# Performance work log

Hardware: AMD Instinct MI355X
Metric: run time of the kernel (lower is better)

## Reference

```python
import jax, jax.numpy as jnp
import numpy as np

N = 160000          # n_users + n_entities (amazon-book scale)
E = 5_120_000       # nonzeros in A_in (avg degree 32)
DIMS = [64, 64, 32, 16]  # conv_dim_list 64-32-16 on top of embed_dim 64


def setup_inputs() -> dict:
    key = jax.random.key(0)
    ks = jax.random.split(key, 4 + 4 * (len(DIMS) - 1))
    inp = {
        "ego": jax.random.normal(ks[0], (N, DIMS[0]), dtype=jnp.float32) * 0.1,
        "edge_row": jax.random.randint(ks[1], (E,), 0, N, dtype=jnp.int32),
        "edge_col": jax.random.randint(ks[2], (E,), 0, N, dtype=jnp.int32),
        # normalized-adjacency-like values
        "edge_val": jax.random.uniform(ks[3], (E,), dtype=jnp.float32) / 32.0,
    }
    ki = 4
    for i in range(len(DIMS) - 1):
        din, dout = DIMS[i], DIMS[i + 1]
        scale = 1.0 / np.sqrt(din)
        inp[f"W1_{i}"] = jax.random.normal(ks[ki], (din, dout), dtype=jnp.float32) * scale
        inp[f"b1_{i}"] = jnp.zeros((dout,), dtype=jnp.float32)
        inp[f"W2_{i}"] = jax.random.normal(ks[ki + 1], (din, dout), dtype=jnp.float32) * scale
        inp[f"b2_{i}"] = jnp.zeros((dout,), dtype=jnp.float32)
        ki += 2
    return inp


def _leaky(x):
    return jnp.where(x >= 0, x, 0.01 * x)  # nn.LeakyReLU default slope


def _l2norm(x):
    # F.normalize(x, p=2, dim=1), eps=1e-12
    n = jnp.sqrt(jnp.sum(x * x, axis=1, keepdims=True))
    return x / jnp.maximum(n, 1e-12)


def _spmm(row, col, val, x):
    # sparse A_in (COO) @ x : gather neighbor rows, scale, scatter-add
    msgs = val[:, None] * x[col]                      # [E, d]
    return jax.ops.segment_sum(msgs, row, num_segments=N)  # [N, d]


def reference(ego, edge_row, edge_col, edge_val,
              W1_0, b1_0, W2_0, b2_0,
              W1_1, b1_1, W2_1, b2_1,
              W1_2, b1_2, W2_2, b2_2):
    params = [(W1_0, b1_0, W2_0, b2_0),
              (W1_1, b1_1, W2_1, b2_1),
              (W1_2, b1_2, W2_2, b2_2)]
    x = ego
    all_embed = [x]
    for W1, b1, W2, b2 in params:
        side = _spmm(edge_row, edge_col, edge_val, x)         # A_in @ ego
        sum_emb = _leaky((x + side) @ W1 + b1)                # linear1 branch
        bi_emb = _leaky((x * side) @ W2 + b2)                 # linear2 branch
        x = sum_emb + bi_emb                                  # (dropout = identity, eval)
        all_embed.append(_l2norm(x))
    return jnp.concatenate(all_embed, axis=1)                 # [N, 64+64+32+16]
```

## Files before the change

kernel.cpp:

```cpp
#include <hip/hip_runtime.h>
#include <hip/hip_bf16.h>

#define LEAKY(v) ((v) >= 0.0f ? (v) : 0.01f * (v))

typedef int iv4 __attribute__((ext_vector_type(4)));
typedef unsigned short us4 __attribute__((ext_vector_type(4)));
typedef short s8v __attribute__((ext_vector_type(8)));
typedef float f4 __attribute__((ext_vector_type(4)));

constexpr int SH = 9;
constexpr int RPB = 1 << SH;
constexpr int NBMAX = 320;
constexpr int CHUNK = 6144;

__device__ __forceinline__ unsigned short f2bf(float v) {
  unsigned u = __float_as_uint(v);
  return (unsigned short)((u + 0x7fffu + ((u >> 16) & 1u)) >> 16);
}
__device__ __forceinline__ float bf2f(unsigned short h) {
  return __uint_as_float((unsigned)h << 16);
}

__global__ void k_init(const float* __restrict__ ego, float* __restrict__ out,
                       unsigned short* __restrict__ xh, int n) {
  int tid = blockIdx.x * blockDim.x + threadIdx.x;
  int total = n * 16;
  int stride = gridDim.x * blockDim.x;
  for (int t = tid; t < total; t += stride) {
    int r = t >> 4, c = (t & 15) * 4;
    float4 v = *(const float4*)(ego + (size_t)r * 64 + c);
    *(float4*)(out + (size_t)r * 176 + c) = v;
    if (xh) {
      us4 h;
      h.x = f2bf(v.x); h.y = f2bf(v.y); h.z = f2bf(v.z); h.w = f2bf(v.w);
      *(us4*)(xh + (size_t)r * 64 + c) = h;
    }
  }
}

__global__ void __launch_bounds__(256) k_hist(const int* __restrict__ erow,
                                              int* __restrict__ bcnt, int E, int nb) {
  __shared__ int h[NBMAX];
  for (int i = threadIdx.x; i < NBMAX; i += 256) h[i] = 0;
  __syncthreads();
  int tid = blockIdx.x * blockDim.x + threadIdx.x;
  int stride = gridDim.x * blockDim.x;
  for (int e = tid; e < E; e += stride) atomicAdd(&h[erow[e] >> SH], 1);
  __syncthreads();
  for (int b = threadIdx.x; b < nb; b += 256)
    if (h[b]) atomicAdd(&bcnt[b], h[b]);
}

__global__ void k_scanb(const int* __restrict__ bcnt, int* __restrict__ boff,
                        int* __restrict__ bcur, int* __restrict__ rp,
                        int nb, int n, int E) {
  int l = threadIdx.x;
  constexpr int PB = NBMAX / 64;
  int local[PB];
  int s = 0;
  int base = l * PB;
  for (int j = 0; j < PB; ++j) {
    int b = base + j;
    int c = (b < nb) ? bcnt[b] : 0;
    local[j] = c;
    s += c;
  }
  int incl = s;
  for (int d = 1; d < 64; d <<= 1) {
    int v = __shfl_up(incl, d);
    if (l >= d) incl += v;
  }
  int ex = incl - s;
  for (int j = 0; j < PB; ++j) {
    int b = base + j;
    if (b <= nb) { boff[b] = ex; bcur[b] = ex; }
    ex += local[j];
  }
  if (l == 63) boff[nb] = incl;
  if (l == 0) rp[n] = E;
}

__global__ void __launch_bounds__(256) k_bucket(
    const int* __restrict__ erow, const int* __restrict__ ecol,
    const float* __restrict__ ev, int* __restrict__ bcur,
    int2* __restrict__ bkt, int E, int nb) {
  __shared__ int hist[NBMAX];
  __shared__ int excl[NBMAX + 1];
  __shared__ int curl[NBMAX];
  __shared__ int gbase[NBMAX];
  __shared__ int2 skv[CHUNK];
  int base = blockIdx.x * CHUNK;
  int cnt = min(CHUNK, E - base);

  for (int i = threadIdx.x; i < NBMAX; i += 256) hist[i] = 0;
  __syncthreads();
  for (int i = threadIdx.x; i < cnt; i += 256)
    atomicAdd(&hist[erow[base + i] >> SH], 1);
  __syncthreads();

  if (threadIdx.x < 64) {
    int l = threadIdx.x;
    constexpr int PB = NBMAX / 64;
    int lsum[PB];
    int s = 0;
    for (int j = 0; j < PB; ++j) { lsum[j] = hist[l * PB + j]; s += lsum[j]; }
    int incl = s;
    for (int d = 1; d < 64; d <<= 1) {
      int v = __shfl_up(incl, d);
      if (l >= d) incl += v;
    }
    int ex = incl - s;
    for (int j = 0; j < PB; ++j) { excl[l * PB + j] = ex; ex += lsum[j]; }
    if (l == 63) excl[NBMAX] = incl;
  }
  __syncthreads();

  for (int b = threadIdx.x; b < nb; b += 256) {
    curl[b] = 0;
    int c = hist[b];
    if (c) gbase[b] = atomicAdd(&bcur[b], c);
  }
  __syncthreads();

  for (int i = threadIdx.x; i < cnt; i += 256) {
    int r = erow[base + i];
    int b = r >> SH;
    int lr = r & (RPB - 1);
    int slot = excl[b] + atomicAdd(&curl[b], 1);
    int2 p;
    p.x = (lr << 18) | ecol[base + i];
    p.y = __float_as_int(ev[base + i]);
    skv[slot] = p;
  }
  __syncthreads();

  for (int s = threadIdx.x; s < cnt; s += 256) {
    int lo = 0, hi = nb;
    while (hi - lo > 1) {
      int mid = (lo + hi) >> 1;
      if (excl[mid] <= s) lo = mid; else hi = mid;
    }
    bkt[gbase[lo] + (s - excl[lo])] = skv[s];
  }
}

__global__ void __launch_bounds__(512) k_bsort(
    const int* __restrict__ boff, const int2* __restrict__ bkt,
    int2* __restrict__ cv, int* __restrict__ rp, int n) {
  __shared__ int cnt[RPB];
  __shared__ int sc[RPB];
  __shared__ int exs[RPB];
  __shared__ int cur[RPB];
  int b = blockIdx.x;
  int off = boff[b];
  int m = boff[b + 1] - off;
  int t = threadIdx.x;

  cnt[t] = 0;
  __syncthreads();
  for (int i = t; i < m; i += 512) atomicAdd(&cnt[bkt[off + i].x >> 18], 1);
  __syncthreads();
  sc[t] = cnt[t];
  __syncthreads();
  for (int o = 1; o < RPB; o <<= 1) {
    int v = (t >= o) ? sc[t - o] : 0;
    __syncthreads();
    sc[t] += v;
    __syncthreads();
  }
  int ex = sc[t] - cnt[t];
  exs[t] = ex;
  cur[t] = 0;
  int row = (b << SH) + t;
  if (row < n) rp[row] = off + ex;
  __syncthreads();
  for (int i = t; i < m; i += 512) {
    int2 p = bkt[off + i];
    int lr = p.x >> 18;
    int pos = exs[lr] + atomicAdd(&cur[lr], 1);
    int2 q;
    q.x = p.x & 0x3FFFF;
    q.y = p.y;
    cv[off + pos] = q;
  }
}

template <int DIN, bool BF>
__global__ void __launch_bounds__(256, 8) k_gam(
    const int* __restrict__ rp, const int2* __restrict__ cv,
    const unsigned short* __restrict__ xh, const float* __restrict__ xin,
    unsigned* __restrict__ amp, int n) {
  int row = (int)((blockIdx.x * (unsigned)blockDim.x + threadIdx.x) >> 6);
  int lane = threadIdx.x & 63;
  if (row >= n) return;

  int f = lane & (DIN - 1);
  int beg = rp[row], end = rp[row + 1];

  float xv = (lane < DIN) ? xin[(size_t)row * 176 + lane] : 0.0f;

#define GATH(col) (BF ? bf2f(xh[(unsigned)((col) * 64 + f)]) \
                      : xin[(size_t)(col) * 176 + f])
  float acc = 0.0f;
  int e = beg;
  if ((e & 1) && e < end) {
    int2 q = cv[e];
    acc = fmaf(__int_as_float(q.y), GATH(q.x), acc);
    ++e;
  }
  for (; e + 4 <= end; e += 4) {
    iv4 a = *(const iv4*)(cv + e);
    iv4 b = *(const iv4*)(cv + e + 2);
    float g0 = GATH(a.x);
    float g1 = GATH(a.z);
    float g2 = GATH(b.x);
    float g3 = GATH(b.z);
    acc = fmaf(__int_as_float(a.y), g0, acc);
    acc = fmaf(__int_as_float(a.w), g1, acc);
    acc = fmaf(__int_as_float(b.y), g2, acc);
    acc = fmaf(__int_as_float(b.w), g3, acc);
  }
  for (; e + 2 <= end; e += 2) {
    iv4 a = *(const iv4*)(cv + e);
    float g0 = GATH(a.x);
    float g1 = GATH(a.z);
    acc = fmaf(__int_as_float(a.y), g0, acc);
    acc = fmaf(__int_as_float(a.w), g1, acc);
  }
  if (e < end) {
    int2 q = cv[e];
    acc = fmaf(__int_as_float(q.y), GATH(q.x), acc);
  }
#undef GATH

  if (lane < DIN) {
    float a = xv + acc, m = xv * acc;
    amp[(size_t)row * 64 + lane] = (unsigned)f2bf(a) | ((unsigned)f2bf(m) << 16);
  }
}

template <int DIN, int DOUT>
__global__ void __launch_bounds__(256) k_xf(
    const unsigned* __restrict__ amp,
    const float* __restrict__ W1, const float* __restrict__ b1,
    const float* __restrict__ W2, const float* __restrict__ b2,
    float* __restrict__ outp, unsigned short* __restrict__ xh, int n) {
  constexpr int ROWB = DIN * 2;
  constexpr int RMASK = (ROWB / 16) - 1;
  constexpr int NTC = DOUT / 16;
  __shared__ unsigned short sA[64 * DIN];
  __shared__ unsigned short sM[64 * DIN];
  __shared__ unsigned short sW1[DOUT * DIN];
  __shared__ unsigned short sW2[DOUT * DIN];

  int row0 = blockIdx.x * 64;

  constexpr int PAIRS = DIN / 2;
  for (int i = threadIdx.x; i < 64 * PAIRS; i += 256) {
    int r = i / PAIRS, fp = (i - r * PAIRS) * 2;
    unsigned lo = 0, hi = 0;
    if (row0 + r < n) {
      uint2 q = *(const uint2*)(amp + (size_t)(row0 + r) * 64 + fp);
      lo = (q.x & 0xffffu) | ((q.y & 0xffffu) << 16);
      hi = (q.x >> 16) | (q.y & 0xffff0000u);
    }
    int boff = r * ROWB + ((fp * 2) ^ ((r & RMASK) << 4));
    *(unsigned*)((char*)sA + boff) = lo;
    *(unsigned*)((char*)sM + boff) = hi;
  }
  for (int i = threadIdx.x; i < DIN * DOUT; i += 256) {
    int k = i / DOUT, c = i - k * DOUT;
    int boff = c * ROWB + ((k * 2) ^ ((c & RMASK) << 4));
    *(unsigned short*)((char*)sW1 + boff) = f2bf(W1[i]);
    *(unsigned short*)((char*)sW2 + boff) = f2bf(W2[i]);
  }
  __syncthreads();

  int w = threadIdx.x >> 6, l = threadIdx.x & 63;
  int tr = w;

  f4 acc1[NTC], acc2[NTC];
#pragma unroll
  for (int tc = 0; tc < NTC; ++tc) {
    acc1[tc] = (f4){0.0f, 0.0f, 0.0f, 0.0f};
    acc2[tc] = (f4){0.0f, 0.0f, 0.0f, 0.0f};
  }

#pragma unroll
  for (int k0 = 0; k0 < DIN; k0 += 32) {
    int ra = tr * 16 + (l & 15);
    int inb = (k0 + (l >> 4) * 8) * 2;
    s8v af = *(const s8v*)((const char*)sA + ra * ROWB + (inb ^ ((ra & RMASK) << 4)));
    s8v mf = *(const s8v*)((const char*)sM + ra * ROWB + (inb ^ ((ra & RMASK) << 4)));
#pragma unroll
    for (int tc = 0; tc < NTC; ++tc) {
      int rc = tc * 16 + (l & 15);
      int wb = rc * ROWB + (inb ^ ((rc & RMASK) << 4));
      s8v w1 = *(const s8v*)((const char*)sW1 + wb);
      s8v w2 = *(const s8v*)((const char*)sW2 + wb);
      acc1[tc] = __builtin_amdgcn_mfma_f32_16x16x32_bf16(af, w1, acc1[tc], 0, 0, 0);
      acc2[tc] = __builtin_amdgcn_mfma_f32_16x16x32_bf16(mf, w2, acc2[tc], 0, 0, 0);
    }
  }

#pragma unroll
  for (int tc = 0; tc < NTC; ++tc) {
    int c = tc * 16 + (l & 15);
    float bb1 = b1[c], bb2 = b2[c];
#pragma unroll
    for (int j = 0; j < 4; ++j) {
      int r = tr * 16 + (l >> 4) * 4 + j;
      if (row0 + r < n) {
        float v1 = acc1[tc][j] + bb1;
        float v2 = acc2[tc][j] + bb2;
        float xn = LEAKY(v1) + LEAKY(v2);
        outp[(size_t)(row0 + r) * 176 + c] = xn;
        if (xh) xh[(size_t)(row0 + r) * 64 + c] = f2bf(xn);
      }
    }
  }
}

__global__ void __launch_bounds__(256) k_norm(float* out, int n) {
  int row = (int)((blockIdx.x * (unsigned)blockDim.x + threadIdx.x) >> 6);
  int lane = threadIdx.x & 63;
  if (row >= n) return;
  float* r = out + (size_t)row * 176;
  float a = r[64 + lane];
  float b = (lane < 48) ? r[128 + lane] : 0.0f;
  float sa = a * a;
  float sb_ = (lane < 32) ? b * b : 0.0f;
  float sc = (lane >= 32 && lane < 48) ? b * b : 0.0f;
#pragma unroll
  for (int off = 32; off; off >>= 1) {
    sa += __shfl_xor(sa, off);
    sb_ += __shfl_xor(sb_, off);
    sc += __shfl_xor(sc, off);
  }
  float ia = 1.0f / fmaxf(sqrtf(sa), 1e-12f);
  float ib = 1.0f / fmaxf(sqrtf(sb_), 1e-12f);
  float ic = 1.0f / fmaxf(sqrtf(sc), 1e-12f);
  r[64 + lane] = a * ia;
  if (lane < 48) r[128 + lane] = b * ((lane < 32) ? ib : ic);
}

extern "C" void kernel_launch(void* const* d_in, const int* in_sizes, int n_in,
                              void* d_out, int out_size, void* d_ws, size_t ws_size,
                              hipStream_t stream) {
  const float* ego = (const float*)d_in[0];
  const int* erow = (const int*)d_in[1];
  const int* ecol = (const int*)d_in[2];
  const float* ev = (const float*)d_in[3];
  const int n = in_sizes[0] / 64;
  const int E = in_sizes[1];
  const int nb = (n + RPB - 1) >> SH;

  float* out = (float*)d_out;

  int2* bkt = (int2*)d_ws;
  int2* cv = bkt + E;
  int* rp = (int*)(cv + E);
  int* bcnt = rp + n + 1;
  int* boff = bcnt + NBMAX;
  int* bcur = boff + NBMAX + 1;
  unsigned short* xh = (unsigned short*)(bcur + NBMAX);
  unsigned* amp = (unsigned*)d_ws;

  size_t need_bf = (size_t)((char*)(xh + (size_t)n * 64) - (char*)d_ws);
  bool bf = ws_size >= need_bf;
  unsigned short* xhp = bf ? xh : nullptr;

  const int rblocks = (n + 3) / 4;
  const int xblocks = (n + 63) / 64;

  k_init<<<2048, 256, 0, stream>>>(ego, out, xhp, n);
  hipMemsetAsync(bcnt, 0, NBMAX * sizeof(int), stream);
  k_hist<<<1024, 256, 0, stream>>>(erow, bcnt, E, nb);
  k_scanb<<<1, 64, 0, stream>>>(bcnt, boff, bcur, rp, nb, n, E);
  k_bucket<<<(E + CHUNK - 1) / CHUNK, 256, 0, stream>>>(erow, ecol, ev, bcur, bkt, E, nb);
  k_bsort<<<nb, 512, 0, stream>>>(boff, bkt, cv, rp, n);

  const float* W1_0 = (const float*)d_in[4];
  const float* B1_0 = (const float*)d_in[5];
  const float* W2_0 = (const float*)d_in[6];
  const float* B2_0 = (const float*)d_in[7];
  const float* W1_1 = (const float*)d_in[8];
  const float* B1_1 = (const float*)d_in[9];
  const float* W2_1 = (const float*)d_in[10];
  const float* B2_1 = (const float*)d_in[11];
  const float* W1_2 = (const float*)d_in[12];
  const float* B1_2 = (const float*)d_in[13];
  const float* W2_2 = (const float*)d_in[14];
  const float* B2_2 = (const float*)d_in[15];

  if (bf) {
    k_gam<64, true><<<rblocks, 256, 0, stream>>>(rp, cv, xh, out, amp, n);
    k_xf<64, 64><<<xblocks, 256, 0, stream>>>(amp, W1_0, B1_0, W2_0, B2_0, out + 64, xh, n);
    k_gam<64, true><<<rblocks, 256, 0, stream>>>(rp, cv, xh, out + 64, amp, n);
    k_xf<64, 32><<<xblocks, 256, 0, stream>>>(amp, W1_1, B1_1, W2_1, B2_1, out + 128, xh, n);
    k_gam<32, true><<<rblocks, 256, 0, stream>>>(rp, cv, xh, out + 128, amp, n);
    k_xf<32, 16><<<xblocks, 256, 0, stream>>>(amp, W1_2, B1_2, W2_2, B2_2, out + 160, nullptr, n);
  } else {
    k_gam<64, false><<<rblocks, 256, 0, stream>>>(rp, cv, nullptr, out, amp, n);
    k_xf<64, 64><<<xblocks, 256, 0, stream>>>(amp, W1_0, B1_0, W2_0, B2_0, out + 64, nullptr, n);
    k_gam<64, false><<<rblocks, 256, 0, stream>>>(rp, cv, nullptr, out + 64, amp, n);
    k_xf<64, 32><<<xblocks, 256, 0, stream>>>(amp, W1_1, B1_1, W2_1, B2_1, out + 128, nullptr, n);
    k_gam<32, false><<<rblocks, 256, 0, stream>>>(rp, cv, nullptr, out + 128, amp, n);
    k_xf<32, 16><<<xblocks, 256, 0, stream>>>(amp, W1_2, B1_2, W2_2, B2_2, out + 160, nullptr, n);
  }

  k_norm<<<rblocks, 256, 0, stream>>>(out, n);
}
```

Baseline: 860.8 us.

## Gather bf16 rows with 16-byte vector loads, splitting edges across lanes

For the bf16 gather path, each lane now loads eight bf16 features with one 16-byte load, and a wave handles several edges at once (64/(DIN/8) edges per iteration). Partial sums are then combined with xor shuffles, and the result is written with vectorized stores. The edge index/value for the next iteration is prefetched. This aims to cut the number of load instructions and make better use of memory transactions in the SpMM gather. The cost is shuffle reductions and extra per-lane registers. The fp32 path also drops its 4-way unrolled loop.

New measurement: 759.5 us. 11.8% less time.

```diff
diff --git a/kernel.cpp b/kernel.cpp
--- a/kernel.cpp
+++ b/kernel.cpp
@@ -7,6 +7,8 @@
 typedef unsigned short us4 __attribute__((ext_vector_type(4)));
 typedef short s8v __attribute__((ext_vector_type(8)));
 typedef float f4 __attribute__((ext_vector_type(4)));
+typedef float fv8 __attribute__((ext_vector_type(8)));
+typedef unsigned uv8 __attribute__((ext_vector_type(8)));
 
 constexpr int SH = 9;
 constexpr int RPB = 1 << SH;
@@ -194,48 +196,76 @@
   int lane = threadIdx.x & 63;
   if (row >= n) return;
 
-  int f = lane & (DIN - 1);
   int beg = rp[row], end = rp[row + 1];
 
-  float xv = (lane < DIN) ? xin[(size_t)row * 176 + lane] : 0.0f;
-
-#define GATH(col) (BF ? bf2f(xh[(unsigned)((col) * 64 + f)]) \
-                      : xin[(size_t)(col) * 176 + f])
-  float acc = 0.0f;
-  int e = beg;
-  if ((e & 1) && e < end) {
-    int2 q = cv[e];
-    acc = fmaf(__int_as_float(q.y), GATH(q.x), acc);
-    ++e;
-  }
-  for (; e + 4 <= end; e += 4) {
-    iv4 a = *(const iv4*)(cv + e);
-    iv4 b = *(const iv4*)(cv + e + 2);
-    float g0 = GATH(a.x);
-    float g1 = GATH(a.z);
-    float g2 = GATH(b.x);
-    float g3 = GATH(b.z);
-    acc = fmaf(__int_as_float(a.y), g0, acc);
-    acc = fmaf(__int_as_float(a.w), g1, acc);
-    acc = fmaf(__int_as_float(b.y), g2, acc);
-    acc = fmaf(__int_as_float(b.w), g3, acc);
-  }
-  for (; e + 2 <= end; e += 2) {
-    iv4 a = *(const iv4*)(cv + e);
-    float g0 = GATH(a.x);
-    float g1 = GATH(a.z);
-    acc = fmaf(__int_as_float(a.y), g0, acc);
-    acc = fmaf(__int_as_float(a.w), g1, acc);
-  }
-  if (e < end) {
-    int2 q = cv[e];
-    acc = fmaf(__int_as_float(q.y), GATH(q.x), acc);
-  }
-#undef GATH
-
-  if (lane < DIN) {
-    float a = xv + acc, m = xv * acc;
-    amp[(size_t)row * 64 + lane] = (unsigned)f2bf(a) | ((unsigned)f2bf(m) << 16);
+  if constexpr (BF) {
+    constexpr int LPE = DIN / 8;
+    constexpr int EPI = 64 / LPE;
+    int eg = lane / LPE;
+    int ch = lane % LPE;
+
+    float acc[8];
+#pragma unroll
+    for (int j = 0; j < 8; ++j) acc[j] = 0.0f;
+
+    if (beg < end) {
+      int2 q = cv[min(beg + eg, end - 1)];
+      for (int e = beg; e < end; e += EPI) {
+        int2 qn = cv[min(e + EPI + eg, end - 1)];
+        float val = (e + eg < end) ? __int_as_float(q.y) : 0.0f;
+        s8v xr = *(const s8v*)(xh + (size_t)(unsigned)q.x * 64 + ch * 8);
+#pragma unroll
+        for (int j = 0; j < 4; ++j) {
+          unsigned d = ((const unsigned*)&xr)[j];
+          acc[2 * j] = fmaf(val, __uint_as_float(d << 16), acc[2 * j]);
+          acc[2 * j + 1] = fmaf(val, __uint_as_float(d & 0xffff0000u), acc[2 * j + 1]);
+        }
+        q = qn;
+      }
+    }
+
+#pragma unroll
+    for (int off = LPE; off < 64; off <<= 1) {
+#pragma unroll
+      for (int j = 0; j < 8; ++j) acc[j] += __shfl_xor(acc[j], off);
+    }
+
+    if (lane < LPE) {
+      fv8 xv = *(const fv8*)(xin + (size_t)row * 176 + lane * 8);
+      uv8 w;
+#pragma unroll
+      for (int j = 0; j < 8; ++j) {
+        float a = xv[j] + acc[j];
+        float m = xv[j] * acc[j];
+        w[j] = (unsigned)f2bf(a) | ((unsigned)f2bf(m) << 16);
+      }
+      *(uv8*)(amp + (size_t)row * 64 + lane * 8) = w;
+    }
+  } else {
+    int f = lane & (DIN - 1);
+    float xv = (lane < DIN) ? xin[(size_t)row * 176 + lane] : 0.0f;
+    float acc = 0.0f;
+    int e = beg;
+    if ((e & 1) && e < end) {
+      int2 q = cv[e];
+      acc = fmaf(__int_as_float(q.y), xin[(size_t)(unsigned)q.x * 176 + f], acc);
+      ++e;
+    }
+    for (; e + 2 <= end; e += 2) {
+      iv4 a = *(const iv4*)(cv + e);
+      float g0 = xin[(size_t)(unsigned)a.x * 176 + f];
+      float g1 = xin[(size_t)(unsigned)a.z * 176 + f];
+      acc = fmaf(__int_as_float(a.y), g0, acc);
+      acc = fmaf(__int_as_float(a.w), g1, acc);
+    }
+    if (e < end) {
+      int2 q = cv[e];
+      acc = fmaf(__int_as_float(q.y), xin[(size_t)(unsigned)q.x * 176 + f], acc);
+    }
+    if (lane < DIN) {
+      float a = xv + acc, m = xv * acc;
+      amp[(size_t)row * 64 + lane] = (unsigned)f2bf(a) | ((unsigned)f2bf(m) << 16);
+    }
   }
 }
 
```
